# Optimization experiments

Measured on AMD Instinct MI355X. Metric: run time of the kernel, lower is better.

Reference implementation:

```python
import jax, jax.numpy as jnp
import numpy as np

C = 512
G = 32  # num_norm_groups
EPS = 1e-6


def setup_inputs() -> dict:
    key = jax.random.key(0)
    ks = jax.random.split(key, 10)
    B, H, W = 8, 64, 64
    s = 1.0 / np.sqrt(C)
    return {
        "x": jax.random.normal(ks[0], (B, C, H, W), dtype=jnp.float32),
        "gamma": jnp.ones((C,), jnp.float32),
        "beta": jnp.zeros((C,), jnp.float32),
        "Wq": jax.random.uniform(ks[1], (C, C), jnp.float32, -s, s),
        "bq": jax.random.uniform(ks[2], (C,), jnp.float32, -s, s),
        "Wk": jax.random.uniform(ks[3], (C, C), jnp.float32, -s, s),
        "bk": jax.random.uniform(ks[4], (C,), jnp.float32, -s, s),
        "Wv": jax.random.uniform(ks[5], (C, C), jnp.float32, -s, s),
        "bv": jax.random.uniform(ks[6], (C,), jnp.float32, -s, s),
        "Wo": jax.random.uniform(ks[7], (C, C), jnp.float32, -s, s),
    }


def group_norm(x, gamma, beta):
    # x: [B, C, H, W]; normalize over each group of C//G channels and all spatial dims
    B, Cc, H, W = x.shape
    xg = x.reshape(B, G, Cc // G, H, W)
    mean = jnp.mean(xg, axis=(2, 3, 4), keepdims=True)
    var = jnp.var(xg, axis=(2, 3, 4), keepdims=True)
    xg = (xg - mean) * jax.lax.rsqrt(var + EPS)
    x = xg.reshape(B, Cc, H, W)
    return x * gamma[None, :, None, None] + beta[None, :, None, None]


def reference(x, gamma, beta, Wq, bq, Wk, bk, Wv, bv, Wo):
    B, Cc, H, W = x.shape
    out = group_norm(x, gamma, beta)
    # [B, C, H, W] -> [B, H*W, C]
    out = out.transpose(0, 2, 3, 1).reshape(B, H * W, Cc)
    q = out @ Wq.T + bq
    k = out @ Wk.T + bk
    v = out @ Wv.T + bv
    score = jnp.einsum('bic,bjc->bij', q, k) / jnp.sqrt(jnp.float32(Cc))
    score = jax.nn.softmax(score, axis=-1)
    out = jnp.einsum('bij,bjc->bic', score, v)
    out = out @ Wo.T
    out = out.reshape(B, H, W, Cc).transpose(0, 3, 1, 2)
    return out + x
```

## Files before the change

kernel.cpp:

```cpp
#include <hip/hip_runtime.h>
#include <hip/hip_bf16.h>
#include <cstdint>
#include <cstddef>

typedef __hip_bfloat16 BF;
typedef __attribute__((ext_vector_type(8))) short bhalf8;
typedef __attribute__((ext_vector_type(4))) float floatx4;

#define NB 8
#define NC 512
#define NHW 4096
#define NG 32

__device__ __forceinline__ float b2f(short h) {
    union { unsigned u; float f; } c;
    c.u = ((unsigned)(unsigned short)h) << 16;
    return c.f;
}
__device__ __forceinline__ short f2b(float f) {
    __hip_bfloat16 h = __float2bfloat16(f);
    short s;
    __builtin_memcpy(&s, &h, 2);
    return s;
}

__device__ __forceinline__ void gload16(const BF* g, BF* l) {
    __builtin_amdgcn_global_load_lds(
        (const __attribute__((address_space(1))) void*)g,
        (__attribute__((address_space(3))) void*)l, 16, 0, 0);
}

__global__ __launch_bounds__(256) void f2b_convert(const float* __restrict__ src,
                                                   BF* __restrict__ dst, int n) {
    int i = (blockIdx.x * 256 + threadIdx.x) * 4;
    if (i >= n) return;
    float4 v = *(const float4*)&src[i];
    dst[i]     = __float2bfloat16(v.x);
    dst[i + 1] = __float2bfloat16(v.y);
    dst[i + 2] = __float2bfloat16(v.z);
    dst[i + 3] = __float2bfloat16(v.w);
}

__global__ __launch_bounds__(256) void gn_stats(const float* __restrict__ x,
                                                float* __restrict__ stats) {
    const int bg = blockIdx.x;
    const long base = (long)bg * 65536;
    float s = 0.f, q = 0.f;
    for (int i = threadIdx.x * 4; i < 65536; i += 256 * 4) {
        float4 v4 = *(const float4*)&x[base + i];
        s += v4.x + v4.y + v4.z + v4.w;
        q += v4.x * v4.x + v4.y * v4.y + v4.z * v4.z + v4.w * v4.w;
    }
#pragma unroll
    for (int o = 32; o; o >>= 1) { s += __shfl_down(s, o); q += __shfl_down(q, o); }
    __shared__ float rs[4], rq[4];
    const int w = threadIdx.x >> 6;
    if ((threadIdx.x & 63) == 0) { rs[w] = s; rq[w] = q; }
    __syncthreads();
    if (threadIdx.x == 0) {
        s = rs[0] + rs[1] + rs[2] + rs[3];
        q = rq[0] + rq[1] + rq[2] + rq[3];
        float mean = s * (1.f / 65536.f);
        float var = q * (1.f / 65536.f) - mean * mean;
        stats[2 * bg]     = mean;
        stats[2 * bg + 1] = rsqrtf(fmaxf(var, 0.f) + 1e-6f);
    }
}

__global__ __launch_bounds__(256) void gn_apply(const float* __restrict__ x,
                                                const float* __restrict__ gamma,
                                                const float* __restrict__ beta,
                                                const float* __restrict__ stats,
                                                BF* __restrict__ n) {
    __shared__ float tile[64][65];
    const int b = blockIdx.z, c0 = blockIdx.y * 64, s0 = blockIdx.x * 64;
    const long xbase = ((long)b * NC + c0) * NHW + s0;
#pragma unroll
    for (int i = 0; i < 16; i++) {
        int lin = i * 256 + threadIdx.x;
        int cl = lin >> 6, sl = lin & 63;
        int c = c0 + cl;
        float2 mr = ((const float2*)stats)[b * NG + (c >> 4)];
        float v = x[xbase + (long)cl * NHW + sl];
        v = (v - mr.x) * mr.y * gamma[c] + beta[c];
        tile[cl][sl] = v;
    }
    __syncthreads();
    const long nbase = ((long)b * NHW + s0) * NC + c0;
#pragma unroll
    for (int i = 0; i < 16; i++) {
        int lin = i * 256 + threadIdx.x;
        int sl = lin >> 6, cl = lin & 63;
        n[nbase + (long)sl * NC + cl] = __float2bfloat16(tile[cl][sl]);
    }
}

template <bool BIAS, bool TRANS>
__global__ __launch_bounds__(256, 2) void gemm128(
    const BF* __restrict__ A, long aStride,
    const BF* __restrict__ Bm, long bStride,
    BF* __restrict__ C, long cStride,
    const float* __restrict__ bias,
    int M, int N, int K, float scale)
{
    __shared__ __align__(16) BF sA[128 * 32];
    __shared__ __align__(16) BF sB[128 * 32];
    const int tid = threadIdx.x;
    const int wave = tid >> 6, lane = tid & 63;
    const int bm = blockIdx.y * 128, bn = blockIdx.x * 128;
    const BF* Ab = A + (long)blockIdx.z * aStride + (long)bm * K;
    const BF* Bb = Bm + (long)blockIdx.z * bStride + (long)bn * K;

    const int srow = wave * 32 + (lane >> 2);
    const int sk = (lane & 3) * 8;
    const BF* gA0 = Ab + (long)srow * K + sk;
    const BF* gA1 = gA0 + (long)16 * K;
    const BF* gB0 = Bb + (long)srow * K + sk;
    const BF* gB1 = gB0 + (long)16 * K;
    BF* lA0 = &sA[(wave * 32) * 32];
    BF* lA1 = &sA[(wave * 32 + 16) * 32];
    BF* lB0 = &sB[(wave * 32) * 32];
    BF* lB1 = &sB[(wave * 32 + 16) * 32];

    floatx4 acc[4][4];
#pragma unroll
    for (int i = 0; i < 4; i++)
#pragma unroll
        for (int j = 0; j < 4; j++) acc[i][j] = (floatx4){0.f, 0.f, 0.f, 0.f};

    const int wm = (wave >> 1) * 64, wn = (wave & 1) * 64;
    const int lr = lane & 15, lk = (lane >> 4) * 8;

    for (int k0 = 0; k0 < K; k0 += 32) {
        __syncthreads();
        gload16(gA0 + k0, lA0);
        gload16(gA1 + k0, lA1);
        gload16(gB0 + k0, lB0);
        gload16(gB1 + k0, lB1);
        __syncthreads();
        bhalf8 af[4], bfr[4];
#pragma unroll
        for (int i = 0; i < 4; i++)
            af[i] = *(const bhalf8*)&sA[(wm + i * 16 + lr) * 32 + lk];
#pragma unroll
        for (int i = 0; i < 4; i++)
            bfr[i] = *(const bhalf8*)&sB[(wn + i * 16 + lr) * 32 + lk];
#pragma unroll
        for (int mi = 0; mi < 4; mi++)
#pragma unroll
            for (int ni = 0; ni < 4; ni++)
                acc[mi][ni] = __builtin_amdgcn_mfma_f32_16x16x32_bf16(
                    af[mi], bfr[ni], acc[mi][ni], 0, 0, 0);
    }

    BF* Cb = C + (long)blockIdx.z * cStride;
#pragma unroll
    for (int ni = 0; ni < 4; ni++) {
        const int col = bn + wn + ni * 16 + lr;
        const float bv = BIAS ? bias[col] : 0.0f;
#pragma unroll
        for (int mi = 0; mi < 4; mi++) {
            const int row0 = bm + wm + mi * 16 + (lane >> 4) * 4;
#pragma unroll
            for (int r = 0; r < 4; r++) {
                float v = acc[mi][ni][r] * scale + bv;
                if (TRANS) Cb[(long)col * M + row0 + r] = __float2bfloat16(v);
                else       Cb[(long)(row0 + r) * N + col] = __float2bfloat16(v);
            }
        }
    }
}

__global__ __launch_bounds__(256, 2) void gemm64(
    const BF* __restrict__ A, long aStride,
    const BF* __restrict__ Bm, long bStride,
    BF* __restrict__ C, long cStride,
    int N, int K, float scale)
{
    __shared__ __align__(16) BF sA[64 * 32];
    __shared__ __align__(16) BF sB[128 * 32];
    const int tid = threadIdx.x;
    const int wave = tid >> 6, lane = tid & 63;
    const int bm = blockIdx.y * 64, bn = blockIdx.x * 128;
    const BF* Ab = A + (long)blockIdx.z * aStride + (long)bm * K;
    const BF* Bb = Bm + (long)blockIdx.z * bStride + (long)bn * K;

    const int rowoff = lane >> 2, sk = (lane & 3) * 8;
    const BF* gA0 = Ab + (long)(wave * 16 + rowoff) * K + sk;
    const BF* gB0 = Bb + (long)(wave * 32 + rowoff) * K + sk;
    const BF* gB1 = gB0 + (long)16 * K;
    BF* lA0 = &sA[(wave * 16) * 32];
    BF* lB0 = &sB[(wave * 32) * 32];
    BF* lB1 = &sB[(wave * 32 + 16) * 32];

    floatx4 acc[2][4];
#pragma unroll
    for (int i = 0; i < 2; i++)
#pragma unroll
        for (int j = 0; j < 4; j++) acc[i][j] = (floatx4){0.f, 0.f, 0.f, 0.f};

    const int wm = (wave >> 1) * 32, wn = (wave & 1) * 64;
    const int lr = lane & 15, lk = (lane >> 4) * 8;

    for (int k0 = 0; k0 < K; k0 += 32) {
        __syncthreads();
        gload16(gA0 + k0, lA0);
        gload16(gB0 + k0, lB0);
        gload16(gB1 + k0, lB1);
        __syncthreads();
        bhalf8 af[2], bfr[4];
#pragma unroll
        for (int i = 0; i < 2; i++)
            af[i] = *(const bhalf8*)&sA[(wm + i * 16 + lr) * 32 + lk];
#pragma unroll
        for (int i = 0; i < 4; i++)
            bfr[i] = *(const bhalf8*)&sB[(wn + i * 16 + lr) * 32 + lk];
#pragma unroll
        for (int mi = 0; mi < 2; mi++)
#pragma unroll
            for (int ni = 0; ni < 4; ni++)
                acc[mi][ni] = __builtin_amdgcn_mfma_f32_16x16x32_bf16(
                    af[mi], bfr[ni], acc[mi][ni], 0, 0, 0);
    }

    BF* Cb = C + (long)blockIdx.z * cStride;
#pragma unroll
    for (int ni = 0; ni < 4; ni++) {
        const int col = bn + wn + ni * 16 + lr;
#pragma unroll
        for (int mi = 0; mi < 2; mi++) {
            const int row0 = bm + wm + mi * 16 + (lane >> 4) * 4;
#pragma unroll
            for (int r = 0; r < 4; r++)
                Cb[(long)(row0 + r) * N + col] = __float2bfloat16(acc[mi][ni][r] * scale);
        }
    }
}

__global__ __launch_bounds__(256) void softmax4096(BF* __restrict__ S) {
    const long base = (long)blockIdx.x * 4096 + threadIdx.x * 16;
    const int tid = threadIdx.x, w = tid >> 6;
    bhalf8 u = *(bhalf8*)&S[base];
    bhalf8 u2 = *(bhalf8*)&S[base + 8];
    float v[16];
    float m = -1e30f;
#pragma unroll
    for (int j = 0; j < 8; j++) { v[j] = b2f(u[j]); v[8 + j] = b2f(u2[j]); }
#pragma unroll
    for (int j = 0; j < 16; j++) m = fmaxf(m, v[j]);
#pragma unroll
    for (int o = 32; o; o >>= 1) m = fmaxf(m, __shfl_xor(m, o));
    __shared__ float rm[4], rs[4];
    if ((tid & 63) == 0) rm[w] = m;
    __syncthreads();
    m = fmaxf(fmaxf(rm[0], rm[1]), fmaxf(rm[2], rm[3]));
    float s = 0.f;
#pragma unroll
    for (int j = 0; j < 16; j++) { v[j] = __expf(v[j] - m); s += v[j]; }
#pragma unroll
    for (int o = 32; o; o >>= 1) s += __shfl_xor(s, o);
    if ((tid & 63) == 0) rs[w] = s;
    __syncthreads();
    s = rs[0] + rs[1] + rs[2] + rs[3];
    const float inv = 1.0f / s;
#pragma unroll
    for (int j = 0; j < 8; j++) { u[j] = f2b(v[j] * inv); u2[j] = f2b(v[8 + j] * inv); }
    *(bhalf8*)&S[base] = u;
    *(bhalf8*)&S[base + 8] = u2;
}

__global__ __launch_bounds__(256) void add_residual_T(const BF* __restrict__ fin,
                                                      const float* __restrict__ x,
                                                      float* __restrict__ out) {
    __shared__ float tile[64][65];
    const int b = blockIdx.z, c0 = blockIdx.y * 64, s0 = blockIdx.x * 64;
    const long fbase = ((long)b * NHW + s0) * NC + c0;
#pragma unroll
    for (int i = 0; i < 16; i++) {
        int lin = i * 256 + threadIdx.x;
        int sl = lin >> 6, cl = lin & 63;
        tile[sl][cl] = __bfloat162float(fin[fbase + (long)sl * NC + cl]);
    }
    __syncthreads();
    const long obase = ((long)b * NC + c0) * NHW + s0;
#pragma unroll
    for (int i = 0; i < 16; i++) {
        int lin = i * 256 + threadIdx.x;
        int cl = lin >> 6, sl = lin & 63;
        long a = obase + (long)cl * NHW + sl;
        out[a] = tile[sl][cl] + x[a];
    }
}

extern "C" void kernel_launch(void* const* d_in, const int* in_sizes, int n_in,
                              void* d_out, int out_size, void* d_ws, size_t ws_size,
                              hipStream_t stream) {
    const float* x     = (const float*)d_in[0];
    const float* gamma = (const float*)d_in[1];
    const float* beta  = (const float*)d_in[2];
    const float* Wq    = (const float*)d_in[3];
    const float* bq    = (const float*)d_in[4];
    const float* Wk    = (const float*)d_in[5];
    const float* bk    = (const float*)d_in[6];
    const float* Wv    = (const float*)d_in[7];
    const float* bv    = (const float*)d_in[8];
    const float* Wo    = (const float*)d_in[9];
    float* out = (float*)d_out;

    const long ACTB = (long)NHW * NC;
    const long SB   = (long)NHW * NHW;
    const long WSZ  = (long)NC * NC;

    char* ws = (char*)d_ws;
    float* stats = (float*)ws;
    BF* wb = (BF*)(ws + 4096);
    BF* q  = wb + 4 * WSZ;
    BF* kk = q + NB * ACTB;
    BF* vT = kk + NB * ACTB;
    BF* R  = vT + NB * ACTB;
    BF* n = R;
    BF* S = R;
    BF* fin = R;

    const size_t base_need = 4096ull + (size_t)4 * WSZ * 2 + (size_t)3 * NB * ACTB * 2;
    long sroom = (ws_size > base_need) ? (long)((ws_size - base_need) / (SB * 2)) : 1;
    int chunk = (int)(sroom < 1 ? 1 : (sroom > NB ? NB : sroom));
    while (NB % chunk) chunk--;

    f2b_convert<<<256, 256, 0, stream>>>(Wq, wb + 0 * WSZ, (int)WSZ);
    f2b_convert<<<256, 256, 0, stream>>>(Wk, wb + 1 * WSZ, (int)WSZ);
    f2b_convert<<<256, 256, 0, stream>>>(Wv, wb + 2 * WSZ, (int)WSZ);
    f2b_convert<<<256, 256, 0, stream>>>(Wo, wb + 3 * WSZ, (int)WSZ);

    gn_stats<<<NB * NG, 256, 0, stream>>>(x, stats);
    gn_apply<<<dim3(NHW / 64, NC / 64, NB), 256, 0, stream>>>(x, gamma, beta, stats, n);

    gemm128<true, false><<<dim3(NC / 128, NHW / 128, NB), 256, 0, stream>>>(
        n, ACTB, wb + 0 * WSZ, 0, q, ACTB, bq, NHW, NC, NC, 1.0f);
    gemm128<true, false><<<dim3(NC / 128, NHW / 128, NB), 256, 0, stream>>>(
        n, ACTB, wb + 1 * WSZ, 0, kk, ACTB, bk, NHW, NC, NC, 1.0f);
    gemm128<true, true><<<dim3(NC / 128, NHW / 128, NB), 256, 0, stream>>>(
        n, ACTB, wb + 2 * WSZ, 0, vT, ACTB, bv, NHW, NC, NC, 1.0f);

    const float iscl = 0.044194173824159216f;
    for (int b0 = 0; b0 < NB; b0 += chunk) {
        gemm128<false, false><<<dim3(NHW / 128, NHW / 128, chunk), 256, 0, stream>>>(
            q + b0 * ACTB, ACTB, kk + b0 * ACTB, ACTB, S, SB, nullptr,
            NHW, NHW, NC, iscl);
        softmax4096<<<NHW * chunk, 256, 0, stream>>>(S);
        if (chunk >= 4)
            gemm128<false, false><<<dim3(NC / 128, NHW / 128, chunk), 256, 0, stream>>>(
                S, SB, vT + b0 * ACTB, ACTB, q + b0 * ACTB, ACTB, nullptr,
                NHW, NC, NHW, 1.0f);
        else
            gemm64<<<dim3(NC / 128, NHW / 64, chunk), 256, 0, stream>>>(
                S, SB, vT + b0 * ACTB, ACTB, q + b0 * ACTB, ACTB, NC, NHW, 1.0f);
    }

    gemm128<false, false><<<dim3(NC / 128, NHW / 128, NB), 256, 0, stream>>>(
        q, ACTB, wb + 3 * WSZ, 0, fin, ACTB, nullptr, NHW, NC, NC, 1.0f);

    add_residual_T<<<dim3(NHW / 64, NC / 64, NB), 256, 0, stream>>>(fin, x, out);
}
```

Measured before the change: 889.5 us.

## Fuse QKV GEMMs, fuse Wo GEMM with residual transpose, add full-width PV kernel

The three Q/K/V projection GEMMs are merged into one launch over the concatenated weights, with the epilogue choosing the destination and the transposed store for V. The output projection writes fp32 directly in channel-major layout and adds the residual, which removes the separate add_residual_T kernel and the bf16 intermediate round trip. A new PV kernel computes all 512 output channels per block of 32 query rows, so each score tile is read from memory once instead of four times. The main risks are strided, uncoalesced writes in the fused epilogues and heavy shared-memory loads of V per block.

```diff
diff --git a/kernel.cpp b/kernel.cpp
--- a/kernel.cpp
+++ b/kernel.cpp
@@ -95,12 +95,10 @@
     }
 }
 
-template <bool BIAS, bool TRANS>
-__global__ __launch_bounds__(256, 2) void gemm128(
+__global__ __launch_bounds__(256, 3) void sgemm(
     const BF* __restrict__ A, long aStride,
     const BF* __restrict__ Bm, long bStride,
     BF* __restrict__ C, long cStride,
-    const float* __restrict__ bias,
     int M, int N, int K, float scale)
 {
     __shared__ __align__(16) BF sA[128 * 32];
@@ -157,82 +155,231 @@
 #pragma unroll
     for (int ni = 0; ni < 4; ni++) {
         const int col = bn + wn + ni * 16 + lr;
-        const float bv = BIAS ? bias[col] : 0.0f;
 #pragma unroll
         for (int mi = 0; mi < 4; mi++) {
             const int row0 = bm + wm + mi * 16 + (lane >> 4) * 4;
 #pragma unroll
-            for (int r = 0; r < 4; r++) {
-                float v = acc[mi][ni][r] * scale + bv;
-                if (TRANS) Cb[(long)col * M + row0 + r] = __float2bfloat16(v);
-                else       Cb[(long)(row0 + r) * N + col] = __float2bfloat16(v);
-            }
+            for (int r = 0; r < 4; r++)
+                Cb[(long)(row0 + r) * N + col] = __float2bfloat16(acc[mi][ni][r] * scale);
         }
     }
 }
 
-__global__ __launch_bounds__(256, 2) void gemm64(
-    const BF* __restrict__ A, long aStride,
-    const BF* __restrict__ Bm, long bStride,
-    BF* __restrict__ C, long cStride,
-    int N, int K, float scale)
+__global__ __launch_bounds__(256, 3) void qkv_gemm(
+    const BF* __restrict__ A, const BF* __restrict__ Bm,
+    BF* __restrict__ q, BF* __restrict__ kk, BF* __restrict__ vT,
+    const float* __restrict__ bq, const float* __restrict__ bk,
+    const float* __restrict__ bv)
 {
-    __shared__ __align__(16) BF sA[64 * 32];
+    const int K = NC;
+    __shared__ __align__(16) BF sA[128 * 32];
     __shared__ __align__(16) BF sB[128 * 32];
     const int tid = threadIdx.x;
     const int wave = tid >> 6, lane = tid & 63;
-    const int bm = blockIdx.y * 64, bn = blockIdx.x * 128;
-    const BF* Ab = A + (long)blockIdx.z * aStride + (long)bm * K;
-    const BF* Bb = Bm + (long)blockIdx.z * bStride + (long)bn * K;
-
-    const int rowoff = lane >> 2, sk = (lane & 3) * 8;
-    const BF* gA0 = Ab + (long)(wave * 16 + rowoff) * K + sk;
-    const BF* gB0 = Bb + (long)(wave * 32 + rowoff) * K + sk;
+    const int bm = blockIdx.y * 128, bn = blockIdx.x * 128;
+    const long ACTB = (long)NHW * NC;
+    const BF* Ab = A + blockIdx.z * ACTB + (long)bm * K;
+    const BF* Bb = Bm + (long)bn * K;
+
+    const int srow = wave * 32 + (lane >> 2);
+    const int sk = (lane & 3) * 8;
+    const BF* gA0 = Ab + (long)srow * K + sk;
+    const BF* gA1 = gA0 + (long)16 * K;
+    const BF* gB0 = Bb + (long)srow * K + sk;
     const BF* gB1 = gB0 + (long)16 * K;
-    BF* lA0 = &sA[(wave * 16) * 32];
+    BF* lA0 = &sA[(wave * 32) * 32];
+    BF* lA1 = &sA[(wave * 32 + 16) * 32];
     BF* lB0 = &sB[(wave * 32) * 32];
     BF* lB1 = &sB[(wave * 32 + 16) * 32];
 
-    floatx4 acc[2][4];
-#pragma unroll
-    for (int i = 0; i < 2; i++)
+    floatx4 acc[4][4];
+#pragma unroll
+    for (int i = 0; i < 4; i++)
 #pragma unroll
         for (int j = 0; j < 4; j++) acc[i][j] = (floatx4){0.f, 0.f, 0.f, 0.f};
 
-    const int wm = (wave >> 1) * 32, wn = (wave & 1) * 64;
+    const int wm = (wave >> 1) * 64, wn = (wave & 1) * 64;
     const int lr = lane & 15, lk = (lane >> 4) * 8;
 
     for (int k0 = 0; k0 < K; k0 += 32) {
         __syncthreads();
         gload16(gA0 + k0, lA0);
+        gload16(gA1 + k0, lA1);
         gload16(gB0 + k0, lB0);
         gload16(gB1 + k0, lB1);
         __syncthreads();
-        bhalf8 af[2], bfr[4];
-#pragma unroll
-        for (int i = 0; i < 2; i++)
+        bhalf8 af[4], bfr[4];
+#pragma unroll
+        for (int i = 0; i < 4; i++)
             af[i] = *(const bhalf8*)&sA[(wm + i * 16 + lr) * 32 + lk];
 #pragma unroll
         for (int i = 0; i < 4; i++)
             bfr[i] = *(const bhalf8*)&sB[(wn + i * 16 + lr) * 32 + lk];
 #pragma unroll
-        for (int mi = 0; mi < 2; mi++)
+        for (int mi = 0; mi < 4; mi++)
 #pragma unroll
             for (int ni = 0; ni < 4; ni++)
                 acc[mi][ni] = __builtin_amdgcn_mfma_f32_16x16x32_bf16(
                     af[mi], bfr[ni], acc[mi][ni], 0, 0, 0);
     }
 
-    BF* Cb = C + (long)blockIdx.z * cStride;
+    const int sec = bn >> 9;
+    const float* bp = (sec == 0) ? bq : (sec == 1) ? bk : bv;
+    BF* dst = (sec == 0) ? q : (sec == 1) ? kk : vT;
+    dst += blockIdx.z * ACTB;
+    const int cb = bn & 511;
+#pragma unroll
+    for (int ni = 0; ni < 4; ni++) {
+        const int col = cb + wn + ni * 16 + lr;
+        const float bias = bp[col];
+#pragma unroll
+        for (int mi = 0; mi < 4; mi++) {
+            const int row0 = bm + wm + mi * 16 + (lane >> 4) * 4;
+#pragma unroll
+            for (int r = 0; r < 4; r++) {
+                float v = acc[mi][ni][r] + bias;
+                if (sec == 2) dst[(long)col * NHW + row0 + r] = __float2bfloat16(v);
+                else          dst[(long)(row0 + r) * NC + col] = __float2bfloat16(v);
+            }
+        }
+    }
+}
+
+__global__ __launch_bounds__(256, 3) void wo_gemm(
+    const BF* __restrict__ A, const BF* __restrict__ Bm,
+    const float* __restrict__ x, float* __restrict__ out)
+{
+    const int K = NC;
+    __shared__ __align__(16) BF sA[128 * 32];
+    __shared__ __align__(16) BF sB[128 * 32];
+    const int tid = threadIdx.x;
+    const int wave = tid >> 6, lane = tid & 63;
+    const int bm = blockIdx.y * 128, bn = blockIdx.x * 128;
+    const long ACTB = (long)NHW * NC;
+    const BF* Ab = A + blockIdx.z * ACTB + (long)bm * K;
+    const BF* Bb = Bm + (long)bn * K;
+
+    const int srow = wave * 32 + (lane >> 2);
+    const int sk = (lane & 3) * 8;
+    const BF* gA0 = Ab + (long)srow * K + sk;
+    const BF* gA1 = gA0 + (long)16 * K;
+    const BF* gB0 = Bb + (long)srow * K + sk;
+    const BF* gB1 = gB0 + (long)16 * K;
+    BF* lA0 = &sA[(wave * 32) * 32];
+    BF* lA1 = &sA[(wave * 32 + 16) * 32];
+    BF* lB0 = &sB[(wave * 32) * 32];
+    BF* lB1 = &sB[(wave * 32 + 16) * 32];
+
+    floatx4 acc[4][4];
+#pragma unroll
+    for (int i = 0; i < 4; i++)
+#pragma unroll
+        for (int j = 0; j < 4; j++) acc[i][j] = (floatx4){0.f, 0.f, 0.f, 0.f};
+
+    const int wm = (wave >> 1) * 64, wn = (wave & 1) * 64;
+    const int lr = lane & 15, lk = (lane >> 4) * 8;
+
+    for (int k0 = 0; k0 < K; k0 += 32) {
+        __syncthreads();
+        gload16(gA0 + k0, lA0);
+        gload16(gA1 + k0, lA1);
+        gload16(gB0 + k0, lB0);
+        gload16(gB1 + k0, lB1);
+        __syncthreads();
+        bhalf8 af[4], bfr[4];
+#pragma unroll
+        for (int i = 0; i < 4; i++)
+            af[i] = *(const bhalf8*)&sA[(wm + i * 16 + lr) * 32 + lk];
+#pragma unroll
+        for (int i = 0; i < 4; i++)
+            bfr[i] = *(const bhalf8*)&sB[(wn + i * 16 + lr) * 32 + lk];
+#pragma unroll
+        for (int mi = 0; mi < 4; mi++)
+#pragma unroll
+            for (int ni = 0; ni < 4; ni++)
+                acc[mi][ni] = __builtin_amdgcn_mfma_f32_16x16x32_bf16(
+                    af[mi], bfr[ni], acc[mi][ni], 0, 0, 0);
+    }
+
+    const float* xb = x + blockIdx.z * ACTB;
+    float* ob = out + blockIdx.z * ACTB;
 #pragma unroll
     for (int ni = 0; ni < 4; ni++) {
         const int col = bn + wn + ni * 16 + lr;
 #pragma unroll
+        for (int mi = 0; mi < 4; mi++) {
+            const int row0 = bm + wm + mi * 16 + (lane >> 4) * 4;
+            const long a = (long)col * NHW + row0;
+            float4 xr = *(const float4*)&xb[a];
+            float4 o;
+            o.x = acc[mi][ni][0] + xr.x;
+            o.y = acc[mi][ni][1] + xr.y;
+            o.z = acc[mi][ni][2] + xr.z;
+            o.w = acc[mi][ni][3] + xr.w;
+            *(float4*)&ob[a] = o;
+        }
+    }
+}
+
+__global__ __launch_bounds__(256, 2) void pv512(
+    const BF* __restrict__ S, const BF* __restrict__ vT,
+    BF* __restrict__ attn)
+{
+    __shared__ __align__(16) BF sA[32 * 32];
+    __shared__ __align__(16) BF sB[512 * 32];
+    const int tid = threadIdx.x;
+    const int wave = tid >> 6, lane = tid & 63;
+    const int bm = blockIdx.x * 32;
+    const long SB = (long)NHW * NHW, ACTB = (long)NHW * NC;
+    const BF* Sb = S + blockIdx.y * SB + (long)bm * NHW;
+    const BF* Vb = vT + blockIdx.y * ACTB;
+    BF* Ab = attn + blockIdx.y * ACTB + (long)bm * NC;
+
+    const int rowoff = lane >> 2, sk = (lane & 3) * 8;
+    const BF* gA = Sb + (long)(wave * 16 + rowoff) * NHW + sk;
+    BF* lA = &sA[(wave * 16) * 32];
+    const BF* gB = Vb + (long)(wave * 128 + rowoff) * NHW + sk;
+    BF* lB = &sB[(wave * 128) * 32];
+
+    floatx4 acc[2][8];
+#pragma unroll
+    for (int i = 0; i < 2; i++)
+#pragma unroll
+        for (int j = 0; j < 8; j++) acc[i][j] = (floatx4){0.f, 0.f, 0.f, 0.f};
+
+    const int lr = lane & 15, lk = (lane >> 4) * 8;
+
+    for (int j0 = 0; j0 < NHW; j0 += 32) {
+        __syncthreads();
+        if (wave < 2) gload16(gA + j0, lA);
+#pragma unroll
+        for (int it = 0; it < 8; it++)
+            gload16(gB + (long)it * 16 * NHW + j0, lB + it * 16 * 32);
+        __syncthreads();
+        bhalf8 af[2], bfr[8];
+#pragma unroll
+        for (int i = 0; i < 2; i++)
+            af[i] = *(const bhalf8*)&sA[(i * 16 + lr) * 32 + lk];
+#pragma unroll
+        for (int i = 0; i < 8; i++)
+            bfr[i] = *(const bhalf8*)&sB[(wave * 128 + i * 16 + lr) * 32 + lk];
+#pragma unroll
+        for (int mi = 0; mi < 2; mi++)
+#pragma unroll
+            for (int ni = 0; ni < 8; ni++)
+                acc[mi][ni] = __builtin_amdgcn_mfma_f32_16x16x32_bf16(
+                    af[mi], bfr[ni], acc[mi][ni], 0, 0, 0);
+    }
+
+#pragma unroll
+    for (int ni = 0; ni < 8; ni++) {
+        const int col = wave * 128 + ni * 16 + lr;
+#pragma unroll
         for (int mi = 0; mi < 2; mi++) {
-            const int row0 = bm + wm + mi * 16 + (lane >> 4) * 4;
+            const int row0 = mi * 16 + (lane >> 4) * 4;
 #pragma unroll
             for (int r = 0; r < 4; r++)
-                Cb[(long)(row0 + r) * N + col] = __float2bfloat16(acc[mi][ni][r] * scale);
+                Ab[(long)(row0 + r) * NC + col] = __float2bfloat16(acc[mi][ni][r]);
         }
     }
 }
@@ -267,29 +414,6 @@
     for (int j = 0; j < 8; j++) { u[j] = f2b(v[j] * inv); u2[j] = f2b(v[8 + j] * inv); }
     *(bhalf8*)&S[base] = u;
     *(bhalf8*)&S[base + 8] = u2;
-}
-
-__global__ __launch_bounds__(256) void add_residual_T(const BF* __restrict__ fin,
-                                                      const float* __restrict__ x,
-                                                      float* __restrict__ out) {
-    __shared__ float tile[64][65];
-    const int b = blockIdx.z, c0 = blockIdx.y * 64, s0 = blockIdx.x * 64;
-    const long fbase = ((long)b * NHW + s0) * NC + c0;
-#pragma unroll
-    for (int i = 0; i < 16; i++) {
-        int lin = i * 256 + threadIdx.x;
-        int sl = lin >> 6, cl = lin & 63;
-        tile[sl][cl] = __bfloat162float(fin[fbase + (long)sl * NC + cl]);
-    }
-    __syncthreads();
-    const long obase = ((long)b * NC + c0) * NHW + s0;
-#pragma unroll
-    for (int i = 0; i < 16; i++) {
-        int lin = i * 256 + threadIdx.x;
-        int cl = lin >> 6, sl = lin & 63;
-        long a = obase + (long)cl * NHW + sl;
-        out[a] = tile[sl][cl] + x[a];
-    }
 }
 
 extern "C" void kernel_launch(void* const* d_in, const int* in_sizes, int n_in,
@@ -320,7 +444,6 @@
     BF* R  = vT + NB * ACTB;
     BF* n = R;
     BF* S = R;
-    BF* fin = R;
 
     const size_t base_need = 4096ull + (size_t)4 * WSZ * 2 + (size_t)3 * NB * ACTB * 2;
     long sroom = (ws_size > base_need) ? (long)((ws_size - base_need) / (SB * 2)) : 1;
@@ -335,30 +458,19 @@
     gn_stats<<<NB * NG, 256, 0, stream>>>(x, stats);
     gn_apply<<<dim3(NHW / 64, NC / 64, NB), 256, 0, stream>>>(x, gamma, beta, stats, n);
 
-    gemm128<true, false><<<dim3(NC / 128, NHW / 128, NB), 256, 0, stream>>>(
-        n, ACTB, wb + 0 * WSZ, 0, q, ACTB, bq, NHW, NC, NC, 1.0f);
-    gemm128<true, false><<<dim3(NC / 128, NHW / 128, NB), 256, 0, stream>>>(
-        n, ACTB, wb + 1 * WSZ, 0, kk, ACTB, bk, NHW, NC, NC, 1.0f);
-    gemm128<true, true><<<dim3(NC / 128, NHW / 128, NB), 256, 0, stream>>>(
-        n, ACTB, wb + 2 * WSZ, 0, vT, ACTB, bv, NHW, NC, NC, 1.0f);
+    qkv_gemm<<<dim3(12, NHW / 128, NB), 256, 0, stream>>>(
+        n, wb, q, kk, vT, bq, bk, bv);
 
     const float iscl = 0.044194173824159216f;
     for (int b0 = 0; b0 < NB; b0 += chunk) {
-        gemm128<false, false><<<dim3(NHW / 128, NHW / 128, chunk), 256, 0, stream>>>(
-            q + b0 * ACTB, ACTB, kk + b0 * ACTB, ACTB, S, SB, nullptr,
+        sgemm<<<dim3(NHW / 128, NHW / 128, chunk), 256, 0, stream>>>(
+            q + b0 * ACTB, ACTB, kk + b0 * ACTB, ACTB, S, SB,
             NHW, NHW, NC, iscl);
         softmax4096<<<NHW * chunk, 256, 0, stream>>>(S);
-        if (chunk >= 4)
-            gemm128<false, false><<<dim3(NC / 128, NHW / 128, chunk), 256, 0, stream>>>(
-                S, SB, vT + b0 * ACTB, ACTB, q + b0 * ACTB, ACTB, nullptr,
-                NHW, NC, NHW, 1.0f);
-        else
-            gemm64<<<dim3(NC / 128, NHW / 64, chunk), 256, 0, stream>>>(
-                S, SB, vT + b0 * ACTB, ACTB, q + b0 * ACTB, ACTB, NC, NHW, 1.0f);
-    }
-
-    gemm128<false, false><<<dim3(NC / 128, NHW / 128, NB), 256, 0, stream>>>(
-        q, ACTB, wb + 3 * WSZ, 0, fin, ACTB, nullptr, NHW, NC, NC, 1.0f);
-
-    add_residual_T<<<dim3(NHW / 64, NC / 64, NB), 256, 0, stream>>>(fin, x, out);
-}
+        pv512<<<dim3(NHW / 32, chunk), 256, 0, stream>>>(
+            S, vT + b0 * ACTB, q + b0 * ACTB);
+    }
+
+    wo_gemm<<<dim3(NC / 128, NHW / 128, NB), 256, 0, stream>>>(
+        q, wb + 3 * WSZ, x, out);
+}
```

New measurement: 985.7 us. 10.8% more time.
